# Performance work log

Hardware: AMD Instinct MI355X
Metric: run time of the kernel (lower is better)

The kernel has to match this reference:

```python
import jax, jax.numpy as jnp
import numpy as np

WS = 16       # window size
SHIFT = 8     # shift size
HEADS = 16
DIM = 512
HIDDEN = 2048
B, H, W = 8, 64, 64
EPS = 1e-5


def _rel_coords_table(ws):
    h = np.arange(-(ws - 1), ws, dtype=np.float32)
    t = np.stack(np.meshgrid(h, h, indexing='ij'), axis=-1)  # (2ws-1, 2ws-1, 2)
    t = t / (ws - 1) * 8.0
    t = np.sign(t) * np.log2(np.abs(t) + 1.0) / np.log2(8.0)
    return t.reshape(-1, 2)


def _rel_pos_index(ws):
    coords = np.stack(np.meshgrid(np.arange(ws), np.arange(ws), indexing='ij'))
    cf = coords.reshape(2, -1)                      # (2, N)
    rel = (cf[:, :, None] - cf[:, None, :]).transpose(1, 2, 0)  # (N, N, 2)
    rel[..., 0] += ws - 1
    rel[..., 1] += ws - 1
    rel[..., 0] *= 2 * ws - 1
    return rel.sum(-1)                              # (N, N)


def _attn_mask(h, w, ws, shift):
    img = np.zeros((h, w))
    cnt = 0
    for hs in (slice(0, -ws), slice(-ws, -shift), slice(-shift, None)):
        for wsl in (slice(0, -ws), slice(-ws, -shift), slice(-shift, None)):
            img[hs, wsl] = cnt
            cnt += 1
    mw = img.reshape(h // ws, ws, w // ws, ws).transpose(0, 2, 1, 3).reshape(-1, ws * ws)
    am = mw[:, None, :] - mw[:, :, None]            # (nW, N, N)
    return np.where(am != 0, -100.0, 0.0).astype(np.float32)


def _ln(x, g, b):
    m = x.mean(-1, keepdims=True)
    v = ((x - m) ** 2).mean(-1, keepdims=True)
    return (x - m) * jax.lax.rsqrt(v + EPS) * g + b


def setup_inputs() -> dict:
    key = jax.random.key(0)
    ks = jax.random.split(key, 16)
    s = 0.02
    return {
        'x': jax.random.normal(ks[0], (B, H, W, DIM), jnp.float32),
        'qkv_w': jax.random.normal(ks[1], (3 * DIM, DIM), jnp.float32) * s,
        'q_bias': jnp.zeros((DIM,), jnp.float32),
        'v_bias': jnp.zeros((DIM,), jnp.float32),
        'logit_scale': jnp.full((HEADS, 1, 1), np.log(10.0), jnp.float32),
        'cpb_w1': jax.random.normal(ks[2], (512, 2), jnp.float32) * s,
        'cpb_b1': jnp.zeros((512,), jnp.float32),
        'cpb_w2': jax.random.normal(ks[3], (HEADS, 512), jnp.float32) * s,
        'proj_w': jax.random.normal(ks[4], (DIM, DIM), jnp.float32) * s,
        'proj_b': jnp.zeros((DIM,), jnp.float32),
        'norm1_g': jnp.ones((DIM,), jnp.float32),
        'norm1_b': jnp.zeros((DIM,), jnp.float32),
        'norm2_g': jnp.ones((DIM,), jnp.float32),
        'norm2_b': jnp.zeros((DIM,), jnp.float32),
        'fc1_w': jax.random.normal(ks[5], (HIDDEN, DIM), jnp.float32) * s,
        'fc1_b': jnp.zeros((HIDDEN,), jnp.float32),
        'fc2_w': jax.random.normal(ks[6], (DIM, HIDDEN), jnp.float32) * s,
        'fc2_b': jnp.zeros((DIM,), jnp.float32),
    }


def reference(x, qkv_w, q_bias, v_bias, logit_scale, cpb_w1, cpb_b1, cpb_w2,
              proj_w, proj_b, norm1_g, norm1_b, norm2_g, norm2_b,
              fc1_w, fc1_b, fc2_w, fc2_b):
    b, h, w, c = x.shape
    N = WS * WS
    nW = (h // WS) * (w // WS)
    hd = c // HEADS

    # --- shifted window cosine attention ---
    shifted = jnp.roll(x, (-SHIFT, -SHIFT), axis=(1, 2))
    xw = shifted.reshape(b, h // WS, WS, w // WS, WS, c)
    xw = xw.transpose(0, 1, 3, 2, 4, 5).reshape(-1, N, c)  # (b*nW, N, C)

    bias = jnp.concatenate([q_bias, jnp.zeros_like(q_bias), v_bias])
    qkv = (xw @ qkv_w.T + bias).reshape(-1, N, 3, HEADS, hd).transpose(2, 0, 3, 1, 4)
    q, k, v = qkv[0], qkv[1], qkv[2]  # (Bn, heads, N, hd)

    qn = q / jnp.maximum(jnp.linalg.norm(q, axis=-1, keepdims=True), 1e-12)
    kn = k / jnp.maximum(jnp.linalg.norm(k, axis=-1, keepdims=True), 1e-12)
    scale = jnp.exp(jnp.minimum(logit_scale, jnp.log(jnp.float32(100.0))))  # (heads,1,1)
    attn = jnp.einsum('bhnd,bhmd->bhnm', qn, kn) * scale

    # continuous relative position bias (CPB MLP)
    table = jnp.asarray(_rel_coords_table(WS))                    # (M, 2)
    t = jax.nn.relu(table @ cpb_w1.T + cpb_b1) @ cpb_w2.T          # (M, heads)
    idx = _rel_pos_index(WS).reshape(-1)
    rpb = t[idx].reshape(N, N, HEADS).transpose(2, 0, 1)
    rpb = 16.0 * jax.nn.sigmoid(rpb)
    attn = attn + rpb[None]

    mask = jnp.asarray(_attn_mask(h, w, WS, SHIFT))                # (nW, N, N)
    attn = attn.reshape(b, nW, HEADS, N, N) + mask[None, :, None]
    attn = jax.nn.softmax(attn.reshape(-1, HEADS, N, N), axis=-1)

    out = jnp.einsum('bhnm,bhmd->bhnd', attn, v).transpose(0, 2, 1, 3).reshape(-1, N, c)
    out = out @ proj_w.T + proj_b

    out = out.reshape(b, h // WS, w // WS, WS, WS, c)
    out = out.transpose(0, 1, 3, 2, 4, 5).reshape(b, h, w, c)
    out = jnp.roll(out, (SHIFT, SHIFT), axis=(1, 2))

    # post-norm residuals (SwinV2 style)
    x = x + _ln(out, norm1_g, norm1_b)
    hmid = jax.nn.gelu(x @ fc1_w.T + fc1_b, approximate=False)
    mlp_out = hmid @ fc2_w.T + fc2_b
    x = x + _ln(mlp_out, norm2_g, norm2_b)
    return x
```

## Files before the change

kernel.cpp:

```cpp
#include <hip/hip_runtime.h>
#include <math.h>


#define HEADS 16
#define HD 32
#define NTOK 256
#define DIMC 512
#define HIDDEN 2048

typedef __attribute__((ext_vector_type(8))) short bf16x8;
typedef __attribute__((ext_vector_type(4))) float f32x4;
typedef __attribute__((ext_vector_type(8))) unsigned short ushort8;

#define MFMA16(a, b, c) __builtin_amdgcn_mfma_f32_16x16x32_bf16((a), (b), (c), 0, 0, 0)
#define WAIT_VM(N) asm volatile("s_waitcnt vmcnt(" #N ")" ::: "memory")
#define WAIT_LGKM0 asm volatile("s_waitcnt lgkmcnt(0)" ::: "memory")

__device__ __forceinline__ unsigned short f2bf(float f) {
  union { float f; unsigned u; } v; v.f = f;
  unsigned r = v.u + 0x7FFFu + ((v.u >> 16) & 1u);
  return (unsigned short)(r >> 16);
}
__device__ __forceinline__ float bf2f(unsigned short h) {
  union { unsigned u; float f; } v; v.u = ((unsigned)h) << 16; return v.f;
}
__device__ __forceinline__ void gload16(const void* g, void* l) {
  __builtin_amdgcn_global_load_lds(
      (const __attribute__((address_space(1))) unsigned int*)g,
      (__attribute__((address_space(3))) unsigned int*)l, 16, 0, 0);
}
__device__ __forceinline__ bf16x8 ds_read128(const unsigned short* p) {
  unsigned off = (unsigned)(size_t)(const __attribute__((address_space(3))) unsigned short*)p;
  bf16x8 r;
  asm volatile("ds_read_b128 %0, %1" : "=v"(r) : "v"(off));
  return r;
}
__device__ __forceinline__ int band(int x) { return x < 48 ? 0 : (x < 56 ? 1 : 2); }

__device__ __forceinline__ float gelu_fast(float x) {
  float u2 = x * (1.5957691216f + 0.0713548163f * x * x);
  u2 = fminf(u2, 80.f);
  float e = __expf(u2);
  return x * (e / (e + 1.f));
}

__device__ __forceinline__ void gemm256_main(const unsigned short* Ab, const unsigned short* Bb,
                                             int K, unsigned short* aT, unsigned short* bT,
                                             f32x4 (&acc)[8][4]) {
  const int tid = threadIdx.x;
  const int w = tid >> 6, lane = tid & 63;
  const int cl = lane & 15, g = lane >> 4;
  const int wr = (w >> 2) * 128, wc = (w & 3) * 64;
  const int off0 = (2 * w) * 1024 + lane * 16;
  const int off1 = (2 * w + 1) * 1024 + lane * 16;
  const int r0 = off0 >> 6, c0 = ((off0 >> 4) & 3) ^ ((r0 >> 1) & 3);
  const int r1 = off1 >> 6, c1 = ((off1 >> 4) & 3) ^ ((r1 >> 1) & 3);
  const char* Ac = (const char*)Ab;
  const char* Bc = (const char*)Bb;
  const size_t sA0 = (size_t)r0 * (K * 2) + (size_t)c0 * 16;
  const size_t sA1 = (size_t)r1 * (K * 2) + (size_t)c1 * 16;
  const int T = K >> 5;
#pragma unroll
  for (int p = 0; p < 3; p++) {
    size_t kb = (size_t)p * 64;
    int bo = p * 16384;
    gload16(Ac + sA0 + kb, (char*)aT + bo + off0);
    gload16(Ac + sA1 + kb, (char*)aT + bo + off1);
    gload16(Bc + sA0 + kb, (char*)bT + bo + off0);
    gload16(Bc + sA1 + kb, (char*)bT + bo + off1);
  }
  for (int t = 0; t < T; t++) {
    if (t + 3 <= T) WAIT_VM(8);
    else if (t + 2 == T) WAIT_VM(4);
    else WAIT_VM(0);
    __builtin_amdgcn_s_barrier();
    const int cur = (t & 3) * 8192;
    bf16x8 bfv[4], af[4];
#pragma unroll
    for (int ni = 0; ni < 4; ni++) {
      int row = wc + ni * 16 + cl;
      bfv[ni] = ds_read128(bT + cur + row * 32 + ((g ^ ((row >> 1) & 3)) * 8));
    }
#pragma unroll
    for (int mi = 0; mi < 4; mi++) {
      int row = wr + mi * 16 + cl;
      af[mi] = ds_read128(aT + cur + row * 32 + ((g ^ ((row >> 1) & 3)) * 8));
    }
    if (t + 3 < T) {
      size_t kb = (size_t)(t + 3) * 64;
      int bo = ((t + 3) & 3) * 16384;
      gload16(Ac + sA0 + kb, (char*)aT + bo + off0);
      gload16(Ac + sA1 + kb, (char*)aT + bo + off1);
    }
    WAIT_LGKM0;
    __builtin_amdgcn_sched_barrier(0);
    __builtin_amdgcn_s_setprio(1);
#pragma unroll
    for (int mi = 0; mi < 4; mi++)
#pragma unroll
      for (int ni = 0; ni < 4; ni++) acc[mi][ni] = MFMA16(af[mi], bfv[ni], acc[mi][ni]);
    __builtin_amdgcn_sched_barrier(0);
    __builtin_amdgcn_s_setprio(0);
    __builtin_amdgcn_s_barrier();
    bf16x8 af2[4];
#pragma unroll
    for (int mi = 0; mi < 4; mi++) {
      int row = wr + 64 + mi * 16 + cl;
      af2[mi] = ds_read128(aT + cur + row * 32 + ((g ^ ((row >> 1) & 3)) * 8));
    }
    if (t + 3 < T) {
      size_t kb = (size_t)(t + 3) * 64;
      int bo = ((t + 3) & 3) * 16384;
      gload16(Bc + sA0 + kb, (char*)bT + bo + off0);
      gload16(Bc + sA1 + kb, (char*)bT + bo + off1);
    }
    WAIT_LGKM0;
    __builtin_amdgcn_sched_barrier(0);
    __builtin_amdgcn_s_setprio(1);
#pragma unroll
    for (int mi = 0; mi < 4; mi++)
#pragma unroll
      for (int ni = 0; ni < 4; ni++) acc[4 + mi][ni] = MFMA16(af2[mi], bfv[ni], acc[4 + mi][ni]);
    __builtin_amdgcn_sched_barrier(0);
    __builtin_amdgcn_s_setprio(0);
    __builtin_amdgcn_s_barrier();
  }
}

__device__ __forceinline__ void xcd_swizzle(int& bm, int& bn) {
  int gy = gridDim.y;
  int nwg = gridDim.x * gy;
  int flat = blockIdx.y * gridDim.x + blockIdx.x;
  int cpx = nwg >> 3;
  int swz = (flat & 7) * cpx + (flat >> 3);
  bm = swz / gy;
  bn = swz % gy;
}

__global__ __launch_bounds__(512, 2) void gemm_qkv(const unsigned short* A,
                                                   const unsigned short* Bw, const float* qbias,
                                                   const float* vbias, unsigned short* qo,
                                                   unsigned short* ko, unsigned short* vo) {
  __shared__ unsigned short aT[4 * 8192];
  __shared__ unsigned short bT[4 * 8192];
  int bm, bn;
  xcd_swizzle(bm, bn);
  f32x4 acc[8][4] = {};
  gemm256_main(A + (size_t)bm * 256 * DIMC, Bw + (size_t)bn * 256 * DIMC, DIMC, aT, bT, acc);
  int lane = threadIdx.x & 63, w = threadIdx.x >> 6;
  int wr = (w >> 2) * 128, wc = (w & 3) * 64, g = lane >> 4, cl = lane & 15;
  int which = bn >> 1;
  unsigned short* base = which == 0 ? qo : (which == 1 ? ko : vo);
#pragma unroll
  for (int ni = 0; ni < 4; ni++) {
    int gn = bn * 256 + wc + ni * 16 + cl;
    int wn = gn & 511, head = wn >> 5, hd = wn & 31;
    float bv = (which == 0) ? qbias[wn] : (which == 2 ? vbias[wn] : 0.f);
#pragma unroll
    for (int mi = 0; mi < 8; mi++) {
#pragma unroll
      for (int reg = 0; reg < 4; reg++) {
        int gm = bm * 256 + wr + mi * 16 + 4 * g + reg;
        int win = gm >> 8, tok = gm & 255;
        base[(((size_t)(win * HEADS + head)) * NTOK + tok) * HD + hd] =
            f2bf(acc[mi][ni][reg] + bv);
      }
    }
  }
}

template <int GELU>
__global__ __launch_bounds__(512, 2) void gemm_epi(const unsigned short* A,
                                                   const unsigned short* Bw, const float* bias,
                                                   unsigned short* out, int N, int K) {
  __shared__ unsigned short aT[4 * 8192];
  __shared__ unsigned short bT[4 * 8192];
  int bm, bn;
  xcd_swizzle(bm, bn);
  f32x4 acc[8][4] = {};
  gemm256_main(A + (size_t)bm * 256 * K, Bw + (size_t)bn * 256 * K, K, aT, bT, acc);
  int lane = threadIdx.x & 63, w = threadIdx.x >> 6;
  int wr = (w >> 2) * 128, wc = (w & 3) * 64, g = lane >> 4, cl = lane & 15;
  float bv[4];
#pragma unroll
  for (int ni = 0; ni < 4; ni++) bv[ni] = bias[bn * 256 + wc + ni * 16 + cl];
#pragma unroll
  for (int mi = 0; mi < 8; mi++) {
#pragma unroll
    for (int reg = 0; reg < 4; reg++) {
      int gm = bm * 256 + wr + mi * 16 + 4 * g + reg;
      unsigned short* rowp = out + (size_t)gm * N + bn * 256 + wc + cl;
#pragma unroll
      for (int ni = 0; ni < 4; ni++) {
        float val = acc[mi][ni][reg] + bv[ni];
        if (GELU) val = gelu_fast(val);
        rowp[ni * 16] = f2bf(val);
      }
    }
  }
}

__global__ __launch_bounds__(256) void attn_kernel(const unsigned short* qg,
                                                   const unsigned short* kg,
                                                   const unsigned short* vg, const float* rpbt,
                                                   const float* logit_scale,
                                                   unsigned short* attn_out) {
  __shared__ unsigned short kS[256 * 32];
  __shared__ unsigned short vT[32 * 256];
  __shared__ unsigned short pS[64 * 256];

  int bid = blockIdx.x;
  int qb = bid & 3, h = (bid >> 2) & 15, win = bid >> 6;
  int tid = threadIdx.x, lane = tid & 63, w = tid >> 6;
  int g = lane >> 4, cl = lane & 15;
  const size_t whbase = ((size_t)(win * HEADS + h)) * NTOK * HD;
  const unsigned short* qwin = qg + whbase + (size_t)qb * 64 * HD;
  const unsigned short* kwin = kg + whbase;
  const unsigned short* vwin = vg + whbase;

#pragma unroll
  for (int i = 0; i < 4; i++) {
    int ci = i * 256 + tid, row = ci >> 2, gc = ci & 3;
    uint4 d = *(const uint4*)(kwin + row * 32 + gc * 8);
    *(uint4*)(kS + row * 32 + ((gc ^ ((row >> 1) & 3)) * 8)) = d;
  }
  {
    int tok = tid;
    ushort8 t0 = *(const ushort8*)(vwin + tok * 32);
    ushort8 t1 = *(const ushort8*)(vwin + tok * 32 + 8);
    ushort8 t2 = *(const ushort8*)(vwin + tok * 32 + 16);
    ushort8 t3 = *(const ushort8*)(vwin + tok * 32 + 24);
    int kc = tok >> 3, ki = tok & 7;
#pragma unroll
    for (int j = 0; j < 8; j++) {
      vT[(j)*256 + ((kc ^ (j & 7)) << 3) + ki] = t0[j];
      vT[(8 + j) * 256 + ((kc ^ ((8 + j) & 7)) << 3) + ki] = t1[j];
      vT[(16 + j) * 256 + ((kc ^ ((16 + j) & 7)) << 3) + ki] = t2[j];
      vT[(24 + j) * 256 + ((kc ^ ((24 + j) & 7)) << 3) + ki] = t3[j];
    }
  }
  __syncthreads();

  float scale = __expf(fminf(logit_scale[h], 4.6051702f));

  {
    int row = tid;
    int sw = (row >> 1) & 3;
    ushort8 ch[4];
#pragma unroll
    for (int gc = 0; gc < 4; gc++) ch[gc] = *(const ushort8*)(kS + row * 32 + ((gc ^ sw) * 8));
    float ss = 0.f;
#pragma unroll
    for (int gc = 0; gc < 4; gc++)
#pragma unroll
      for (int j = 0; j < 8; j++) { float f = bf2f(ch[gc][j]); ss += f * f; }
    float rn = rsqrtf(fmaxf(ss, 1e-24f));
#pragma unroll
    for (int gc = 0; gc < 4; gc++) {
      ushort8 o;
#pragma unroll
      for (int j = 0; j < 8; j++) o[j] = f2bf(bf2f(ch[gc][j]) * rn);
      *(ushort8*)(kS + row * 32 + ((gc ^ sw) * 8)) = o;
    }
  }

  bf16x8 qf;
  {
    int qrow = 16 * w + cl;
    ushort8 qraw = *(const ushort8*)(qwin + qrow * 32 + 8 * g);
    float qe[8];
    float ss = 0.f;
#pragma unroll
    for (int j = 0; j < 8; j++) { qe[j] = bf2f(qraw[j]); ss += qe[j] * qe[j]; }
    ss += __shfl_xor(ss, 16, 64);
    ss += __shfl_xor(ss, 32, 64);
    float rn = rsqrtf(fmaxf(ss, 1e-24f)) * scale;
#pragma unroll
    for (int j = 0; j < 8; j++) qf[j] = (short)f2bf(qe[j] * rn);
  }
  __syncthreads();

  f32x4 acc[16];
#pragma unroll
  for (int ct = 0; ct < 16; ct++) {
    int kr = ct * 16 + cl;
    bf16x8 kf = *(const bf16x8*)(kS + kr * 32 + ((g ^ ((kr >> 1) & 3)) * 8));
    f32x4 z = {0.f, 0.f, 0.f, 0.f};
    acc[ct] = MFMA16(qf, kf, z);
  }

  int wh = (win >> 2) & 3, ww = win & 3;
  int bandcc = band(ww * 16 + cl);
  const float* rpbh = rpbt + h * 961;
  float m4[4];
  int baseidx[4], ridq[4];
#pragma unroll
  for (int reg = 0; reg < 4; reg++) {
    int qrow = qb * 64 + 16 * w + 4 * g + reg;
    int ri = qrow >> 4, ci = qrow & 15;
    ridq[reg] = 3 * band(wh * 16 + ri) + band(ww * 16 + ci);
    baseidx[reg] = (ri + 15) * 31 + (ci + 15 - cl);
    m4[reg] = -1e30f;
  }
#pragma unroll
  for (int ct = 0; ct < 16; ct++) {
    int brc = 3 * band(wh * 16 + ct);
#pragma unroll
    for (int reg = 0; reg < 4; reg++) {
      float v = acc[ct][reg] + rpbh[baseidx[reg] - ct * 31] +
                ((ridq[reg] != (brc + bandcc)) ? -100.f : 0.f);
      acc[ct][reg] = v;
      m4[reg] = fmaxf(m4[reg], v);
    }
  }
#pragma unroll
  for (int reg = 0; reg < 4; reg++) {
#pragma unroll
    for (int o = 1; o < 16; o <<= 1) m4[reg] = fmaxf(m4[reg], __shfl_xor(m4[reg], o, 64));
  }

  float s4[4] = {0.f, 0.f, 0.f, 0.f};
#pragma unroll
  for (int ct = 0; ct < 16; ct++) {
#pragma unroll
    for (int reg = 0; reg < 4; reg++) {
      float p = __expf(acc[ct][reg] - m4[reg]);
      s4[reg] += p;
      int row = 16 * w + 4 * g + reg;
      int c = ct * 16 + cl;
      pS[row * 256 + (((c >> 3) ^ (row & 7)) << 3) + (c & 7)] = f2bf(p);
    }
  }
#pragma unroll
  for (int reg = 0; reg < 4; reg++) {
#pragma unroll
    for (int o = 1; o < 16; o <<= 1) s4[reg] += __shfl_xor(s4[reg], o, 64);
  }

  f32x4 o0 = {0.f, 0.f, 0.f, 0.f}, o1 = {0.f, 0.f, 0.f, 0.f};
  int prow = 16 * w + cl;
#pragma unroll
  for (int ks = 0; ks < 8; ks++) {
    bf16x8 pf = *(const bf16x8*)(pS + prow * 256 + ((((ks * 4 + g)) ^ (prow & 7)) << 3));
    int kc = ks * 4 + g;
    bf16x8 vf0 = *(const bf16x8*)(vT + cl * 256 + ((kc ^ (cl & 7)) << 3));
    bf16x8 vf1 = *(const bf16x8*)(vT + (16 + cl) * 256 + ((kc ^ ((16 + cl) & 7)) << 3));
    o0 = MFMA16(pf, vf0, o0);
    o1 = MFMA16(pf, vf1, o1);
  }

#pragma unroll
  for (int reg = 0; reg < 4; reg++) {
    int row = 16 * w + 4 * g + reg;
    float linv = 1.f / s4[reg];
    size_t tokg = (size_t)win * NTOK + qb * 64 + row;
    attn_out[tokg * DIMC + h * 32 + cl] = f2bf(o0[reg] * linv);
    attn_out[tokg * DIMC + h * 32 + 16 + cl] = f2bf(o1[reg] * linv);
  }
}

__global__ __launch_bounds__(256) void cvt_bf16(const float* src, unsigned short* dst, int n8) {
  int i = blockIdx.x * 256 + threadIdx.x;
  if (i >= n8) return;
  const float* s = src + (size_t)i * 8;
  float4 a = *(const float4*)s, b = *(const float4*)(s + 4);
  ushort8 o;
  o[0] = f2bf(a.x); o[1] = f2bf(a.y); o[2] = f2bf(a.z); o[3] = f2bf(a.w);
  o[4] = f2bf(b.x); o[5] = f2bf(b.y); o[6] = f2bf(b.z); o[7] = f2bf(b.w);
  *(ushort8*)(dst + (size_t)i * 8) = o;
}

__device__ __forceinline__ float cpb_coord(int i) {
  float t = (float)(i - 15) * (8.f / 15.f);
  float s = (t > 0.f) ? 1.f : ((t < 0.f) ? -1.f : 0.f);
  return s * log2f(fabsf(t) + 1.f) * (1.f / 3.f);
}

__global__ __launch_bounds__(256) void cpb_kernel(const float* w1, const float* b1, const float* w2,
                                                  float* rpbt) {
  int i = blockIdx.x * 256 + threadIdx.x;
  if (i >= 961 * 16) return;
  int m = i >> 4, h = i & 15;
  int mi = m / 31, mj = m % 31;
  float c0 = cpb_coord(mi), c1 = cpb_coord(mj);
  float acc = 0.f;
  for (int j = 0; j < 512; j++) {
    float hv = fmaxf(w1[2 * j] * c0 + w1[2 * j + 1] * c1 + b1[j], 0.f);
    acc += hv * w2[h * 512 + j];
  }
  rpbt[h * 961 + m] = 16.f / (1.f + __expf(-acc));
}

__global__ __launch_bounds__(256) void xw_gather(const float* x, unsigned short* xw) {
  int idx = blockIdx.x * 256 + threadIdx.x;
  int m = idx >> 6, chunk = idx & 63;
  int win = m >> 8, tok = m & 255;
  int b = win >> 4, wh = (win >> 2) & 3, ww = win & 3;
  int tr = tok >> 4, tc = tok & 15;
  int sr = (wh * 16 + tr + 8) & 63, sc = (ww * 16 + tc + 8) & 63;
  const float* src = x + ((size_t)((b * 64 + sr) * 64 + sc)) * 512 + chunk * 8;
  float4 a = *(const float4*)src, bq = *(const float4*)(src + 4);
  ushort8 o;
  o[0] = f2bf(a.x); o[1] = f2bf(a.y); o[2] = f2bf(a.z); o[3] = f2bf(a.w);
  o[4] = f2bf(bq.x); o[5] = f2bf(bq.y); o[6] = f2bf(bq.z); o[7] = f2bf(bq.w);
  *(ushort8*)(xw + (size_t)m * 512 + chunk * 8) = o;
}

__global__ __launch_bounds__(256) void ln1_kernel(const unsigned short* pr, const float* x,
                                                  const float* gw, const float* bw,
                                                  unsigned short* x1b) {
  int w = threadIdx.x >> 6, lane = threadIdx.x & 63;
  size_t t = (size_t)blockIdx.x * 4 + w;
  int ti = (int)t;
  int b = ti >> 12, rc = ti & 4095, r = rc >> 6, c = rc & 63;
  int sr = (r + 56) & 63, sc = (c + 56) & 63;
  int win = b * 16 + (sr >> 4) * 4 + (sc >> 4);
  int tok = (sr & 15) * 16 + (sc & 15);
  int ch = lane * 8;
  ushort8 pv = *(const ushort8*)(pr + ((size_t)win * 256 + tok) * 512 + ch);
  float pf[8];
  float s = 0.f, s2 = 0.f;
#pragma unroll
  for (int j = 0; j < 8; j++) { pf[j] = bf2f(pv[j]); s += pf[j]; s2 += pf[j] * pf[j]; }
#pragma unroll
  for (int o = 1; o < 64; o <<= 1) { s += __shfl_xor(s, o, 64); s2 += __shfl_xor(s2, o, 64); }
  float mean = s * (1.f / 512.f);
  float rstd = rsqrtf(s2 * (1.f / 512.f) - mean * mean + 1e-5f);
  const float* xrow = x + t * 512 + ch;
  float4 xa = *(const float4*)xrow, xb = *(const float4*)(xrow + 4);
  float xs[8] = {xa.x, xa.y, xa.z, xa.w, xb.x, xb.y, xb.z, xb.w};
  ushort8 o8;
#pragma unroll
  for (int j = 0; j < 8; j++) {
    float y = (pf[j] - mean) * rstd * gw[ch + j] + bw[ch + j];
    o8[j] = f2bf(xs[j] + y);
  }
  *(ushort8*)(x1b + t * 512 + ch) = o8;
}

__global__ __launch_bounds__(256) void ln2_kernel(const unsigned short* mp,
                                                  const unsigned short* x1b, const float* gw,
                                                  const float* bw, float* out) {
  int w = threadIdx.x >> 6, lane = threadIdx.x & 63;
  size_t t = (size_t)blockIdx.x * 4 + w;
  int ch = lane * 8;
  ushort8 mv = *(const ushort8*)(mp + t * 512 + ch);
  float pf[8];
  float s = 0.f, s2 = 0.f;
#pragma unroll
  for (int j = 0; j < 8; j++) { pf[j] = bf2f(mv[j]); s += pf[j]; s2 += pf[j] * pf[j]; }
#pragma unroll
  for (int o = 1; o < 64; o <<= 1) { s += __shfl_xor(s, o, 64); s2 += __shfl_xor(s2, o, 64); }
  float mean = s * (1.f / 512.f);
  float rstd = rsqrtf(s2 * (1.f / 512.f) - mean * mean + 1e-5f);
  ushort8 xv = *(const ushort8*)(x1b + t * 512 + ch);
  float vals[8];
#pragma unroll
  for (int j = 0; j < 8; j++)
    vals[j] = bf2f(xv[j]) + (pf[j] - mean) * rstd * gw[ch + j] + bw[ch + j];
  *(float4*)(out + t * 512 + ch) = make_float4(vals[0], vals[1], vals[2], vals[3]);
  *(float4*)(out + t * 512 + ch + 4) = make_float4(vals[4], vals[5], vals[6], vals[7]);
}

extern "C" void kernel_launch(void* const* d_in, const int* in_sizes, int n_in, void* d_out,
                              int out_size, void* d_ws, size_t ws_size, hipStream_t stream) {
  (void)in_sizes; (void)n_in; (void)out_size; (void)ws_size;
  const float* x = (const float*)d_in[0];
  const float* qkv_w = (const float*)d_in[1];
  const float* q_bias = (const float*)d_in[2];
  const float* v_bias = (const float*)d_in[3];
  const float* logit_sc = (const float*)d_in[4];
  const float* cpb_w1 = (const float*)d_in[5];
  const float* cpb_b1 = (const float*)d_in[6];
  const float* cpb_w2 = (const float*)d_in[7];
  const float* proj_w = (const float*)d_in[8];
  const float* proj_b = (const float*)d_in[9];
  const float* n1g = (const float*)d_in[10];
  const float* n1b = (const float*)d_in[11];
  const float* n2g = (const float*)d_in[12];
  const float* n2b = (const float*)d_in[13];
  const float* fc1_w = (const float*)d_in[14];
  const float* fc1_b = (const float*)d_in[15];
  const float* fc2_w = (const float*)d_in[16];
  const float* fc2_b = (const float*)d_in[17];

  char* ws = (char*)d_ws;
  unsigned short* wq = (unsigned short*)(ws);
  unsigned short* wp = (unsigned short*)(ws + (2ll << 20));
  unsigned short* w1 = (unsigned short*)(ws + (4ll << 20));
  unsigned short* w2 = (unsigned short*)(ws + (8ll << 20));
  float* rpbt = (float*)(ws + (12ll << 20));
  unsigned short* xw = (unsigned short*)(ws + (16ll << 20));
  unsigned short* qbuf = (unsigned short*)(ws + (48ll << 20));
  unsigned short* kbuf = (unsigned short*)(ws + (80ll << 20));
  unsigned short* vbuf = (unsigned short*)(ws + (112ll << 20));
  unsigned short* projout = (unsigned short*)(ws + (144ll << 20));
  unsigned short* x1b = (unsigned short*)(ws + (176ll << 20));
  unsigned short* hmid = (unsigned short*)(ws + (48ll << 20));
  unsigned short* mlpout = xw;
  float* out = (float*)d_out;

  cvt_bf16<<<dim3(384), dim3(256), 0, stream>>>(qkv_w, wq, 1536 * 512 / 8);
  cvt_bf16<<<dim3(128), dim3(256), 0, stream>>>(proj_w, wp, 512 * 512 / 8);
  cvt_bf16<<<dim3(512), dim3(256), 0, stream>>>(fc1_w, w1, 2048 * 512 / 8);
  cvt_bf16<<<dim3(512), dim3(256), 0, stream>>>(fc2_w, w2, 512 * 2048 / 8);
  cpb_kernel<<<dim3(61), dim3(256), 0, stream>>>(cpb_w1, cpb_b1, cpb_w2, rpbt);
  xw_gather<<<dim3(8192), dim3(256), 0, stream>>>(x, xw);

  gemm_qkv<<<dim3(128, 6), dim3(512), 0, stream>>>(xw, wq, q_bias, v_bias, qbuf, kbuf, vbuf);
  attn_kernel<<<dim3(8192), dim3(256), 0, stream>>>(qbuf, kbuf, vbuf, rpbt, logit_sc, xw);
  gemm_epi<0><<<dim3(128, 2), dim3(512), 0, stream>>>(xw, wp, proj_b, projout, 512, 512);
  ln1_kernel<<<dim3(8192), dim3(256), 0, stream>>>(projout, x, n1g, n1b, x1b);

  gemm_epi<1><<<dim3(128, 8), dim3(512), 0, stream>>>(x1b, w1, fc1_b, hmid, 2048, 512);
  gemm_epi<0><<<dim3(128, 2), dim3(512), 0, stream>>>(hmid, w2, fc2_b, mlpout, 512, 2048);
  ln2_kernel<<<dim3(8192), dim3(256), 0, stream>>>(mlpout, x1b, n2g, n2b, out);
}
```

Measured before the change: 477.4 us.

## Software-pipeline LDS fragment reads and drop mid-iteration barriers in GEMM loop

The shared GEMM main loop now prefetches the next K-tile's A and B LDS fragments at the end of each iteration, right after the wait and barrier for that tile. The two per-iteration barriers and sched_barriers that followed the MFMA blocks are removed, and the swizzled LDS offsets are precomputed outside the loop. The aim is to cut barrier stalls and address arithmetic and to hide LDS read latency behind MFMA work. It relies on the 4-deep ring buffer with prefetch distance 3 to stay race-free with fewer barriers, and it raises register pressure by keeping the fragments live across iterations.

Result: no change. 476.1 us (-0.3%).

```diff
diff --git a/kernel.cpp b/kernel.cpp
--- a/kernel.cpp
+++ b/kernel.cpp
@@ -60,6 +60,16 @@
   const size_t sA0 = (size_t)r0 * (K * 2) + (size_t)c0 * 16;
   const size_t sA1 = (size_t)r1 * (K * 2) + (size_t)c1 * 16;
   const int T = K >> 5;
+  int offB[4], offA0[4], offA1[4];
+#pragma unroll
+  for (int i = 0; i < 4; i++) {
+    int rowb = wc + i * 16 + cl;
+    offB[i] = rowb * 32 + ((g ^ ((rowb >> 1) & 3)) * 8);
+    int rowa = wr + i * 16 + cl;
+    offA0[i] = rowa * 32 + ((g ^ ((rowa >> 1) & 3)) * 8);
+    int rowa1 = wr + 64 + i * 16 + cl;
+    offA1[i] = rowa1 * 32 + ((g ^ ((rowa1 >> 1) & 3)) * 8);
+  }
 #pragma unroll
   for (int p = 0; p < 3; p++) {
     size_t kb = (size_t)p * 64;
@@ -69,23 +79,16 @@
     gload16(Bc + sA0 + kb, (char*)bT + bo + off0);
     gload16(Bc + sA1 + kb, (char*)bT + bo + off1);
   }
+  WAIT_VM(8);
+  __builtin_amdgcn_s_barrier();
+  bf16x8 bfv[4], af[4];
+#pragma unroll
+  for (int ni = 0; ni < 4; ni++) bfv[ni] = ds_read128(bT + offB[ni]);
+#pragma unroll
+  for (int mi = 0; mi < 4; mi++) af[mi] = ds_read128(aT + offA0[mi]);
+
   for (int t = 0; t < T; t++) {
-    if (t + 3 <= T) WAIT_VM(8);
-    else if (t + 2 == T) WAIT_VM(4);
-    else WAIT_VM(0);
-    __builtin_amdgcn_s_barrier();
     const int cur = (t & 3) * 8192;
-    bf16x8 bfv[4], af[4];
-#pragma unroll
-    for (int ni = 0; ni < 4; ni++) {
-      int row = wc + ni * 16 + cl;
-      bfv[ni] = ds_read128(bT + cur + row * 32 + ((g ^ ((row >> 1) & 3)) * 8));
-    }
-#pragma unroll
-    for (int mi = 0; mi < 4; mi++) {
-      int row = wr + mi * 16 + cl;
-      af[mi] = ds_read128(aT + cur + row * 32 + ((g ^ ((row >> 1) & 3)) * 8));
-    }
     if (t + 3 < T) {
       size_t kb = (size_t)(t + 3) * 64;
       int bo = ((t + 3) & 3) * 16384;
@@ -99,15 +102,10 @@
     for (int mi = 0; mi < 4; mi++)
 #pragma unroll
       for (int ni = 0; ni < 4; ni++) acc[mi][ni] = MFMA16(af[mi], bfv[ni], acc[mi][ni]);
-    __builtin_amdgcn_sched_barrier(0);
     __builtin_amdgcn_s_setprio(0);
-    __builtin_amdgcn_s_barrier();
     bf16x8 af2[4];
 #pragma unroll
-    for (int mi = 0; mi < 4; mi++) {
-      int row = wr + 64 + mi * 16 + cl;
-      af2[mi] = ds_read128(aT + cur + row * 32 + ((g ^ ((row >> 1) & 3)) * 8));
-    }
+    for (int mi = 0; mi < 4; mi++) af2[mi] = ds_read128(aT + cur + offA1[mi]);
     if (t + 3 < T) {
       size_t kb = (size_t)(t + 3) * 64;
       int bo = ((t + 3) & 3) * 16384;
@@ -121,9 +119,18 @@
     for (int mi = 0; mi < 4; mi++)
 #pragma unroll
       for (int ni = 0; ni < 4; ni++) acc[4 + mi][ni] = MFMA16(af2[mi], bfv[ni], acc[4 + mi][ni]);
-    __builtin_amdgcn_sched_barrier(0);
     __builtin_amdgcn_s_setprio(0);
-    __builtin_amdgcn_s_barrier();
+    if (t + 1 < T) {
+      if (t + 3 < T) WAIT_VM(8);
+      else if (t + 2 < T) WAIT_VM(4);
+      else WAIT_VM(0);
+      __builtin_amdgcn_s_barrier();
+      const int nxt = ((t + 1) & 3) * 8192;
+#pragma unroll
+      for (int ni = 0; ni < 4; ni++) bfv[ni] = ds_read128(bT + nxt + offB[ni]);
+#pragma unroll
+      for (int mi = 0; mi < 4; mi++) af[mi] = ds_read128(aT + nxt + offA0[mi]);
+    }
   }
 }
 
```
